# Kernel optimization log

Hardware: AMD Instinct MI355X
Metric: run time of the kernel (lower is better)

The kernel has to match this reference:

```python
import jax, jax.numpy as jnp
import numpy as np

N_NODES = 50000
N_EDGES = 640000
HID = 128


def _lin_params(key, out_dim, in_dim):
    kw, kb = jax.random.split(key)
    W = jax.random.normal(kw, (out_dim, in_dim), dtype=jnp.float32) * 0.02
    b = jax.random.normal(kb, (out_dim,), dtype=jnp.float32) * 0.02
    return W, b


def setup_inputs() -> dict:
    key = jax.random.key(0)
    ks = jax.random.split(key, 12)
    x = jax.random.normal(ks[0], (N_NODES, 3), dtype=jnp.float32)
    h = jax.random.normal(ks[1], (N_NODES, HID), dtype=jnp.float32)
    edge_index = jax.random.randint(ks[2], (2, N_EDGES), 0, N_NODES, dtype=jnp.int64)
    # edge_mlp: Linear(2H+1,H) -> SiLU -> Linear(H,H) -> SiLU -> Linear(H,H)
    ew1, eb1 = _lin_params(ks[3], HID, 2 * HID + 1)
    ew2, eb2 = _lin_params(ks[4], HID, HID)
    ew3, eb3 = _lin_params(ks[5], HID, HID)
    # coord_mlp: Linear(H,H) -> SiLU -> Linear(H,1)
    cw1, cb1 = _lin_params(ks[6], HID, HID)
    cw2, cb2 = _lin_params(ks[7], 1, HID)
    # node_mlp: Linear(2H,H) -> SiLU -> Linear(H,H) -> SiLU -> Linear(H,H)
    nw1, nb1 = _lin_params(ks[8], HID, 2 * HID)
    nw2, nb2 = _lin_params(ks[9], HID, HID)
    nw3, nb3 = _lin_params(ks[10], HID, HID)
    return {
        "x": x, "h": h, "edge_index": edge_index,
        "ew1": ew1, "eb1": eb1, "ew2": ew2, "eb2": eb2, "ew3": ew3, "eb3": eb3,
        "cw1": cw1, "cb1": cb1, "cw2": cw2, "cb2": cb2,
        "nw1": nw1, "nb1": nb1, "nw2": nw2, "nb2": nb2, "nw3": nw3, "nb3": nb3,
    }


def _lin(z, W, b):
    return z @ W.T + b


def _mlp3(z, W1, b1, W2, b2, W3, b3):
    z = jax.nn.silu(_lin(z, W1, b1))
    z = jax.nn.silu(_lin(z, W2, b2))
    return _lin(z, W3, b3)


def reference(x, h, edge_index,
              ew1, eb1, ew2, eb2, ew3, eb3,
              cw1, cb1, cw2, cb2,
              nw1, nb1, nw2, nb2, nw3, nb3):
    n = h.shape[0]
    src, dst = edge_index[0], edge_index[1]
    rel = x[src] - x[dst]                                   # [E, 3]
    d2 = jnp.sum(rel * rel, axis=-1, keepdims=True)         # [E, 1]
    e_in = jnp.concatenate([h[src], h[dst], d2], axis=-1)   # [E, 2H+1]
    m_ij = _mlp3(e_in, ew1, eb1, ew2, eb2, ew3, eb3)        # [E, H]
    m_aggr = jax.ops.segment_sum(m_ij, src, num_segments=n)  # [N, H]
    coord_coef = jnp.tanh(_lin(jax.nn.silu(_lin(m_ij, cw1, cb1)), cw2, cb2))  # [E, 1]
    delta_x = jax.ops.segment_sum(rel * coord_coef, src, num_segments=n)      # [N, 3]
    x_out = x + delta_x
    h_out = h + _mlp3(jnp.concatenate([h, m_aggr], axis=-1), nw1, nb1, nw2, nb2, nw3, nb3)
    return (x_out, h_out)
```

## Files before the change

kernel.cpp:

```cpp
#include <hip/hip_runtime.h>
#include <hip/hip_bf16.h>

#define N_NODES 50000
#define N_EDGES 640000
#define HID 128

typedef unsigned short ushort_t;
typedef __attribute__((ext_vector_type(8))) short bf16x8;
typedef __attribute__((ext_vector_type(4))) float f32x4;

#define U_MAGGR 0
#define U_HB    6400000
#define U_W1B   12800000
#define U_W2B   12832768
#define U_W3B   12849152
#define U_C1B   12865536
#define U_N1B   12881920
#define U_N2B   12914688
#define U_N3B   12931072
#define U_W1D2  12947456
#define U_WC    12947712
#define U_BC    12964096

__device__ __forceinline__ float silu_f(float v) {
    const float e = __builtin_amdgcn_exp2f(v * -1.442695041f);
    return v * __builtin_amdgcn_rcpf(1.0f + e);
}

__device__ __forceinline__ ushort_t f2b(float f) {
    __hip_bfloat16 b = __float2bfloat16(f);
    return __builtin_bit_cast(ushort_t, b);
}
__device__ __forceinline__ float b2f(ushort_t u) {
    union { float f; unsigned int i; } v; v.i = ((unsigned int)u) << 16; return v.f;
}
__device__ __forceinline__ float u2f(unsigned int u) {
    union { float f; unsigned int i; } v; v.i = u; return v.f;
}
__device__ __forceinline__ unsigned int pack2(float a, float b) {
    return (unsigned int)f2b(a) | ((unsigned int)f2b(b) << 16);
}
__device__ __forceinline__ void up8(const uint4& u, float* f) {
    f[0] = u2f(u.x << 16); f[1] = u2f(u.x & 0xffff0000u);
    f[2] = u2f(u.y << 16); f[3] = u2f(u.y & 0xffff0000u);
    f[4] = u2f(u.z << 16); f[5] = u2f(u.z & 0xffff0000u);
    f[6] = u2f(u.w << 16); f[7] = u2f(u.w & 0xffff0000u);
}
__device__ __forceinline__ void atom_add_f32(float* p, float v) { unsafeAtomicAdd(p, v); }

__device__ __forceinline__ void atom_pk_bf16(ushort_t* p, unsigned int v) {
#if __has_builtin(__builtin_amdgcn_global_atomic_fadd_v2bf16)
    typedef __attribute__((ext_vector_type(2))) short s2;
    s2 sv = __builtin_bit_cast(s2, v);
    __builtin_amdgcn_global_atomic_fadd_v2bf16((__attribute__((address_space(1))) s2*)p, sv);
#else
    unsigned int* up = (unsigned int*)p;
    unsigned int old = __hip_atomic_load(up, __ATOMIC_RELAXED, __HIP_MEMORY_SCOPE_AGENT), assumed;
    do {
        assumed = old;
        float lo = b2f((ushort_t)(assumed & 0xffff)) + b2f((ushort_t)(v & 0xffff));
        float hi = b2f((ushort_t)(assumed >> 16)) + b2f((ushort_t)(v >> 16));
        unsigned int nv = (unsigned int)f2b(lo) | ((unsigned int)f2b(hi) << 16);
        old = atomicCAS(up, assumed, nv);
    } while (old != assumed);
#endif
}

__global__ void prep_kernel(const float* __restrict__ x, const float* __restrict__ h,
                            const float* __restrict__ ew1, const float* __restrict__ ew2,
                            const float* __restrict__ ew3, const float* __restrict__ cw1,
                            const float* __restrict__ nw1, const float* __restrict__ nw2,
                            const float* __restrict__ nw3,
                            ushort_t* __restrict__ wsu, float* __restrict__ xout) {
    long i = (long)blockIdx.x * 256 + threadIdx.x;
    if (i < 3200000) { ((unsigned int*)(wsu + U_MAGGR))[i] = 0u; return; }
    i -= 3200000;
    if (i < 3200000) { ((unsigned int*)(wsu + U_HB))[i] = pack2(h[2 * i], h[2 * i + 1]); return; }
    i -= 3200000;
    if (i < 32768) {
        const int f = (int)(i >> 7);
        const int k = (int)(i & 127);
        const int src = (f < 128) ? (f * 257 + k) : ((f - 128) * 257 + 128 + k);
        wsu[U_W1B + i] = f2b(ew1[src]);
        return;
    }
    i -= 32768;
    if (i < 16384) { wsu[U_W2B + i] = f2b(ew2[i]); return; }
    i -= 16384;
    if (i < 16384) { wsu[U_W3B + i] = f2b(ew3[i]); return; }
    i -= 16384;
    if (i < 16384) { wsu[U_C1B + i] = f2b(cw1[i]); return; }
    i -= 16384;
    if (i < 32768) { wsu[U_N1B + i] = f2b(nw1[i]); return; }
    i -= 32768;
    if (i < 16384) { wsu[U_N2B + i] = f2b(nw2[i]); return; }
    i -= 16384;
    if (i < 16384) { wsu[U_N3B + i] = f2b(nw3[i]); return; }
    i -= 16384;
    if (i < 128) { ((float*)(wsu + U_W1D2))[i] = ew1[i * 257 + 256]; return; }
    i -= 128;
    if (i < 150000) xout[i] = x[i];
}

__global__ __launch_bounds__(256, 4) void ab_kernel(
    const ushort_t* __restrict__ hb, const ushort_t* __restrict__ wab,
    const float* __restrict__ eb1, ushort_t* __restrict__ abp,
    const ushort_t* __restrict__ c1b, const float* __restrict__ ew3,
    const float* __restrict__ eb3, const float* __restrict__ cb1,
    ushort_t* __restrict__ wcb, float* __restrict__ bcv, int nAB) {
    __shared__ ushort_t sH[16384];
    const int t = threadIdx.x;
    const int lane = t & 63;
    const int wid = t >> 6;
    const int r15 = lane & 15;
    const int khi = lane >> 4;
    const int rhi = khi * 4;

    if ((int)blockIdx.x == nAB) {
        for (int i = t; i < 16384; i += 256) {
            const int m = i >> 7, k = i & 127;
            sH[(k * 128 + m) ^ ((k & 7) << 3)] = f2b(ew3[i]);
        }
        __syncthreads();
#pragma unroll
        for (int kh = 0; kh < 2; ++kh) {
#pragma unroll
            for (int fi = 0; fi < 2; ++fi) {
                const int f0 = wid * 32 + fi * 16;
                const int kc = kh * 64;
                f32x4 acc[4];
#pragma unroll
                for (int ni = 0; ni < 4; ++ni) acc[ni] = (f32x4){0.f, 0.f, 0.f, 0.f};
#pragma unroll
                for (int ks = 0; ks < 4; ++ks) {
                    const bf16x8 a0 = *(const bf16x8*)(c1b + (f0 + r15) * 128 + ks * 32 + khi * 8);
                    bf16x8 b[4];
#pragma unroll
                    for (int ni = 0; ni < 4; ++ni) {
                        const int kk = kc + ni * 16 + r15;
                        b[ni] = *(const bf16x8*)(sH + ((kk * 128 + ks * 32 + khi * 8) ^ ((kk & 7) << 3)));
                    }
#pragma unroll
                    for (int ni = 0; ni < 4; ++ni)
                        acc[ni] = __builtin_amdgcn_mfma_f32_16x16x32_bf16(a0, b[ni], acc[ni], 0, 0, 0);
                }
#pragma unroll
                for (int ni = 0; ni < 4; ++ni) {
                    const int kk = kc + ni * 16 + r15;
#pragma unroll
                    for (int j = 0; j < 4; ++j)
                        wcb[(f0 + rhi + j) * 128 + kk] = f2b(acc[ni][j]);
                }
            }
        }
        {
            const int f = t >> 1, hf = t & 1;
            float s = 0.f;
            const int m0 = hf * 64;
#pragma unroll 8
            for (int m = m0; m < m0 + 64; ++m)
                s = fmaf(b2f(c1b[f * 128 + m]), eb3[m], s);
            s += __shfl_xor(s, 1);
            if (hf == 0) bcv[f] = cb1[f] + s;
        }
        return;
    }

    const int fb = wid * 64;
    const int n0 = blockIdx.x * 64;

    const uint4* hb4 = (const uint4*)hb;
#pragma unroll
    for (int it = 0; it < 4; ++it) {
        const int idx = it * 256 + t;
        const int e = idx >> 4, c = idx & 15;
        const int n = n0 + e;
        uint4 v = make_uint4(0u, 0u, 0u, 0u);
        if (n < N_NODES) v = hb4[(size_t)n * 16 + c];
        const int ui = (e * 128 + c * 8) ^ ((e & 7) << 3);
        *(uint4*)(sH + ui) = v;
    }
    __syncthreads();

    f32x4 acc[4][4];
#pragma unroll
    for (int mi = 0; mi < 4; ++mi)
#pragma unroll
        for (int ni = 0; ni < 4; ++ni) acc[mi][ni] = (f32x4){0.f, 0.f, 0.f, 0.f};
#pragma unroll
    for (int ks = 0; ks < 4; ++ks) {
        bf16x8 a[4];
#pragma unroll
        for (int mi = 0; mi < 4; ++mi)
            a[mi] = *(const bf16x8*)(wab + (fb + mi * 16 + r15) * 128 + ks * 32 + khi * 8);
        bf16x8 b[4];
#pragma unroll
        for (int ni = 0; ni < 4; ++ni) {
            const int e = ni * 16 + r15;
            const int ui = (e * 128 + ks * 32 + khi * 8) ^ ((e & 7) << 3);
            b[ni] = *(const bf16x8*)(sH + ui);
        }
#pragma unroll
        for (int mi = 0; mi < 4; ++mi)
#pragma unroll
            for (int ni = 0; ni < 4; ++ni)
                acc[mi][ni] = __builtin_amdgcn_mfma_f32_16x16x32_bf16(a[mi], b[ni], acc[mi][ni], 0, 0, 0);
    }

#pragma unroll
    for (int mi = 0; mi < 4; ++mi) {
        const int f0 = fb + mi * 16 + rhi;
        float4 bb = make_float4(0.f, 0.f, 0.f, 0.f);
        if (f0 >= 128) bb = *(const float4*)&eb1[f0 - 128];
#pragma unroll
        for (int ni = 0; ni < 4; ++ni) {
            const int n = n0 + ni * 16 + r15;
            if (n < N_NODES) {
                *(uint2*)(abp + (size_t)n * 256 + f0) =
                    make_uint2(pack2(acc[mi][ni][0] + bb.x, acc[mi][ni][1] + bb.y),
                               pack2(acc[mi][ni][2] + bb.z, acc[mi][ni][3] + bb.w));
            }
        }
    }
}

template <bool ACT>
__device__ __forceinline__ void dense128(ushort_t* sE, int srcBase, int dstBase,
                                         const ushort_t* __restrict__ W,
                                         const float* __restrict__ bias,
                                         int r15, int khi, int rhi, int fb) {
    f32x4 acc[4];
#pragma unroll
    for (int ni = 0; ni < 4; ++ni) acc[ni] = (f32x4){0.f, 0.f, 0.f, 0.f};
#pragma unroll
    for (int ks = 0; ks < 4; ++ks) {
        const bf16x8 a0 = *(const bf16x8*)(W + (fb + r15) * 128 + ks * 32 + khi * 8);
        bf16x8 b[4];
#pragma unroll
        for (int ni = 0; ni < 4; ++ni) {
            const int edge = ni * 16 + r15;
            const int ui = (srcBase + edge * 128 + ks * 32 + khi * 8) ^ ((edge & 7) << 3);
            b[ni] = *(const bf16x8*)(sE + ui);
        }
#pragma unroll
        for (int ni = 0; ni < 4; ++ni)
            acc[ni] = __builtin_amdgcn_mfma_f32_16x16x32_bf16(a0, b[ni], acc[ni], 0, 0, 0);
    }
    const float4 bb = *(const float4*)&bias[fb + rhi];
#pragma unroll
    for (int ni = 0; ni < 4; ++ni) {
        const int edge = ni * 16 + r15;
        float v0 = acc[ni][0] + bb.x;
        float v1 = acc[ni][1] + bb.y;
        float v2 = acc[ni][2] + bb.z;
        float v3 = acc[ni][3] + bb.w;
        if (ACT) { v0 = silu_f(v0); v1 = silu_f(v1); v2 = silu_f(v2); v3 = silu_f(v3); }
        const int ui = (dstBase + edge * 128 + fb + rhi) ^ ((edge & 7) << 3);
        *(uint2*)(sE + ui) = make_uint2(pack2(v0, v1), pack2(v2, v3));
    }
}

__global__ __launch_bounds__(512, 8) void edge_kernel(
    const float* __restrict__ x, const ushort_t* __restrict__ ab,
    const int* __restrict__ ei,
    const float* __restrict__ w1d2,
    const ushort_t* __restrict__ w2b, const float* __restrict__ eb2,
    const ushort_t* __restrict__ w3b, const float* __restrict__ eb3,
    const ushort_t* __restrict__ wcb, const float* __restrict__ bcv,
    const float* __restrict__ cw2, const float* __restrict__ cb2,
    float* __restrict__ xout, ushort_t* __restrict__ maggr) {
    __shared__ ushort_t sE[16384];
    __shared__ float srel[64][3];
    __shared__ float sd2[64];
    __shared__ int ssrc[64];
    __shared__ float sPart[8][64];

    const int t = threadIdx.x;
    const int lane = t & 63;
    const int wid = t >> 6;
    const int r15 = lane & 15;
    const int khi = lane >> 4;
    const int rhi = khi * 4;
    const int fb = wid * 16;
    const int e0 = blockIdx.x * 64;

    uint4 va[2], vb[2];
    int ui[2], ee[2];
    {
        const uint4* ab4 = (const uint4*)ab;
#pragma unroll
        for (int it = 0; it < 2; ++it) {
            const int idx = it * 512 + t;
            const int e = idx >> 4, c = idx & 15;
            const int s = ei[e0 + e];
            const int d = ei[N_EDGES + e0 + e];
            va[it] = ab4[(size_t)s * 32 + c];
            vb[it] = ab4[(size_t)d * 32 + 16 + c];
            ee[it] = e;
            ui[it] = (e * 128 + c * 8) ^ ((e & 7) << 3);
        }
    }
    if (t < 64) {
        const int s = ei[e0 + t], d = ei[N_EDGES + e0 + t];
        ssrc[t] = s;
        const float rx = x[3 * s] - x[3 * d];
        const float ry = x[3 * s + 1] - x[3 * d + 1];
        const float rz = x[3 * s + 2] - x[3 * d + 2];
        srel[t][0] = rx; srel[t][1] = ry; srel[t][2] = rz;
        sd2[t] = rx * rx + ry * ry + rz * rz;
    }
    __syncthreads();

#pragma unroll
    for (int it = 0; it < 2; ++it) {
        const int c8 = ((it * 512 + t) & 15) * 8;
        const float4 w0 = *(const float4*)&w1d2[c8];
        const float4 w1 = *(const float4*)&w1d2[c8 + 4];
        const float d2 = sd2[ee[it]];
        float fa[8], fbv[8];
        up8(va[it], fa);
        up8(vb[it], fbv);
        const float v0 = silu_f(fmaf(d2, w0.x, fa[0] + fbv[0]));
        const float v1 = silu_f(fmaf(d2, w0.y, fa[1] + fbv[1]));
        const float v2 = silu_f(fmaf(d2, w0.z, fa[2] + fbv[2]));
        const float v3 = silu_f(fmaf(d2, w0.w, fa[3] + fbv[3]));
        const float v4 = silu_f(fmaf(d2, w1.x, fa[4] + fbv[4]));
        const float v5 = silu_f(fmaf(d2, w1.y, fa[5] + fbv[5]));
        const float v6 = silu_f(fmaf(d2, w1.z, fa[6] + fbv[6]));
        const float v7 = silu_f(fmaf(d2, w1.w, fa[7] + fbv[7]));
        uint4 st;
        st.x = pack2(v0, v1); st.y = pack2(v2, v3);
        st.z = pack2(v4, v5); st.w = pack2(v6, v7);
        *(uint4*)(sE + ui[it]) = st;
    }
    __syncthreads();

    dense128<true>(sE, 0, 8192, w2b, eb2, r15, khi, rhi, fb);
    __syncthreads();

    dense128<false>(sE, 8192, 0, w3b, eb3, r15, khi, rhi, fb);

    {
        f32x4 acc[4];
#pragma unroll
        for (int ni = 0; ni < 4; ++ni) acc[ni] = (f32x4){0.f, 0.f, 0.f, 0.f};
#pragma unroll
        for (int ks = 0; ks < 4; ++ks) {
            const bf16x8 a0 = *(const bf16x8*)(wcb + (fb + r15) * 128 + ks * 32 + khi * 8);
            bf16x8 b[4];
#pragma unroll
            for (int ni = 0; ni < 4; ++ni) {
                const int edge = ni * 16 + r15;
                const int u = (8192 + edge * 128 + ks * 32 + khi * 8) ^ ((edge & 7) << 3);
                b[ni] = *(const bf16x8*)(sE + u);
            }
#pragma unroll
            for (int ni = 0; ni < 4; ++ni)
                acc[ni] = __builtin_amdgcn_mfma_f32_16x16x32_bf16(a0, b[ni], acc[ni], 0, 0, 0);
        }
        const float4 bb = *(const float4*)&bcv[fb + rhi];
        const float4 cw = *(const float4*)&cw2[fb + rhi];
        float p[4];
#pragma unroll
        for (int ni = 0; ni < 4; ++ni) {
            float s = silu_f(acc[ni][0] + bb.x) * cw.x;
            s = fmaf(silu_f(acc[ni][1] + bb.y), cw.y, s);
            s = fmaf(silu_f(acc[ni][2] + bb.z), cw.z, s);
            s = fmaf(silu_f(acc[ni][3] + bb.w), cw.w, s);
            p[ni] = s;
        }
#pragma unroll
        for (int ni = 0; ni < 4; ++ni) {
            p[ni] += __shfl_xor(p[ni], 16);
            p[ni] += __shfl_xor(p[ni], 32);
        }
        if (khi == 0) {
#pragma unroll
            for (int ni = 0; ni < 4; ++ni) sPart[wid][ni * 16 + r15] = p[ni];
        }
    }
    __syncthreads();

    {
        unsigned int v[8];
        size_t gaddr[8];
#pragma unroll
        for (int it = 0; it < 8; ++it) {
            const int idx = it * 512 + t;
            const int e = idx >> 6;
            const int dw = idx & 63;
            const int u = (e * 128 + dw * 2) ^ ((e & 7) << 3);
            v[it] = *(const unsigned int*)(sE + u);
            gaddr[it] = (size_t)ssrc[e] * 128 + dw * 2;
        }
#pragma unroll
        for (int it = 0; it < 8; ++it) atom_pk_bf16(maggr + gaddr[it], v[it]);
    }
    if (t < 64) {
        float s = sPart[0][t];
#pragma unroll
        for (int w = 1; w < 8; ++w) s += sPart[w][t];
        const float coef = tanhf(s + cb2[0]);
        const int sn = ssrc[t];
        atom_add_f32(&xout[3 * sn + 0], srel[t][0] * coef);
        atom_add_f32(&xout[3 * sn + 1], srel[t][1] * coef);
        atom_add_f32(&xout[3 * sn + 2], srel[t][2] * coef);
    }
}

__global__ __launch_bounds__(256, 4) void node_kernel(
    const float* __restrict__ h, const ushort_t* __restrict__ hb,
    const ushort_t* __restrict__ maggr,
    const ushort_t* __restrict__ n1b, const float* __restrict__ nb1,
    const ushort_t* __restrict__ n2b, const float* __restrict__ nb2,
    const ushort_t* __restrict__ n3b, const float* __restrict__ nb3,
    float* __restrict__ hout) {
    __shared__ ushort_t sE[16384];
    const int t = threadIdx.x;
    const int lane = t & 63;
    const int wid = t >> 6;
    const int r15 = lane & 15;
    const int khi = lane >> 4;
    const int rhi = khi * 4;
    const int fb = wid * 32;
    const int n0 = blockIdx.x * 64;

    const uint4* hb4 = (const uint4*)hb;
    const uint4* mg4 = (const uint4*)maggr;
#pragma unroll
    for (int it = 0; it < 8; ++it) {
        const int idx = it * 256 + t;
        const int e = idx >> 5, c = idx & 31;
        const int n = n0 + e;
        uint4 v = make_uint4(0u, 0u, 0u, 0u);
        if (n < N_NODES) v = (c < 16) ? hb4[(size_t)n * 16 + c] : mg4[(size_t)n * 16 + (c - 16)];
        const int ui = (e * 256 + c * 8) ^ ((e & 7) << 3);
        *(uint4*)(sE + ui) = v;
    }
    __syncthreads();

    f32x4 acc[2][4];
#pragma unroll
    for (int mi = 0; mi < 2; ++mi)
#pragma unroll
        for (int ni = 0; ni < 4; ++ni) acc[mi][ni] = (f32x4){0.f, 0.f, 0.f, 0.f};
#pragma unroll
    for (int ks = 0; ks < 8; ++ks) {
        const bf16x8 a0 = *(const bf16x8*)(n1b + (fb + r15) * 256 + ks * 32 + khi * 8);
        const bf16x8 a1 = *(const bf16x8*)(n1b + (fb + 16 + r15) * 256 + ks * 32 + khi * 8);
        bf16x8 b[4];
#pragma unroll
        for (int ni = 0; ni < 4; ++ni) {
            const int edge = ni * 16 + r15;
            const int ui = (edge * 256 + ks * 32 + khi * 8) ^ ((edge & 7) << 3);
            b[ni] = *(const bf16x8*)(sE + ui);
        }
#pragma unroll
        for (int ni = 0; ni < 4; ++ni) {
            acc[0][ni] = __builtin_amdgcn_mfma_f32_16x16x32_bf16(a0, b[ni], acc[0][ni], 0, 0, 0);
            acc[1][ni] = __builtin_amdgcn_mfma_f32_16x16x32_bf16(a1, b[ni], acc[1][ni], 0, 0, 0);
        }
    }
    __syncthreads();
    {
        const float4 bb0 = *(const float4*)&nb1[fb + rhi];
        const float4 bb1 = *(const float4*)&nb1[fb + 16 + rhi];
#pragma unroll
        for (int mi = 0; mi < 2; ++mi) {
            const float4 bb = mi ? bb1 : bb0;
#pragma unroll
            for (int ni = 0; ni < 4; ++ni) {
                const int edge = ni * 16 + r15;
                const float v0 = silu_f(acc[mi][ni][0] + bb.x);
                const float v1 = silu_f(acc[mi][ni][1] + bb.y);
                const float v2 = silu_f(acc[mi][ni][2] + bb.z);
                const float v3 = silu_f(acc[mi][ni][3] + bb.w);
                const int ui = (edge * 128 + fb + mi * 16 + rhi) ^ ((edge & 7) << 3);
                *(uint2*)(sE + ui) = make_uint2(pack2(v0, v1), pack2(v2, v3));
            }
        }
    }
    __syncthreads();

    {
#pragma unroll
        for (int half = 0; half < 2; ++half) {
            f32x4 a2[4];
#pragma unroll
            for (int ni = 0; ni < 4; ++ni) a2[ni] = (f32x4){0.f, 0.f, 0.f, 0.f};
            const int fbh = fb + half * 16;
#pragma unroll
            for (int ks = 0; ks < 4; ++ks) {
                const bf16x8 a0 = *(const bf16x8*)(n2b + (fbh + r15) * 128 + ks * 32 + khi * 8);
                bf16x8 b[4];
#pragma unroll
                for (int ni = 0; ni < 4; ++ni) {
                    const int edge = ni * 16 + r15;
                    const int ui = (edge * 128 + ks * 32 + khi * 8) ^ ((edge & 7) << 3);
                    b[ni] = *(const bf16x8*)(sE + ui);
                }
#pragma unroll
                for (int ni = 0; ni < 4; ++ni)
                    a2[ni] = __builtin_amdgcn_mfma_f32_16x16x32_bf16(a0, b[ni], a2[ni], 0, 0, 0);
            }
            const float4 bb = *(const float4*)&nb2[fbh + rhi];
#pragma unroll
            for (int ni = 0; ni < 4; ++ni) {
                const int edge = ni * 16 + r15;
                const float v0 = silu_f(a2[ni][0] + bb.x);
                const float v1 = silu_f(a2[ni][1] + bb.y);
                const float v2 = silu_f(a2[ni][2] + bb.z);
                const float v3 = silu_f(a2[ni][3] + bb.w);
                const int ui = (8192 + edge * 128 + fbh + rhi) ^ ((edge & 7) << 3);
                *(uint2*)(sE + ui) = make_uint2(pack2(v0, v1), pack2(v2, v3));
            }
        }
    }
    __syncthreads();

    {
        f32x4 a3[2][4];
#pragma unroll
        for (int mi = 0; mi < 2; ++mi)
#pragma unroll
            for (int ni = 0; ni < 4; ++ni) a3[mi][ni] = (f32x4){0.f, 0.f, 0.f, 0.f};
#pragma unroll
        for (int ks = 0; ks < 4; ++ks) {
            const bf16x8 a0 = *(const bf16x8*)(n3b + (fb + r15) * 128 + ks * 32 + khi * 8);
            const bf16x8 a1 = *(const bf16x8*)(n3b + (fb + 16 + r15) * 128 + ks * 32 + khi * 8);
            bf16x8 b[4];
#pragma unroll
            for (int ni = 0; ni < 4; ++ni) {
                const int edge = ni * 16 + r15;
                const int ui = (8192 + edge * 128 + ks * 32 + khi * 8) ^ ((edge & 7) << 3);
                b[ni] = *(const bf16x8*)(sE + ui);
            }
#pragma unroll
            for (int ni = 0; ni < 4; ++ni) {
                a3[0][ni] = __builtin_amdgcn_mfma_f32_16x16x32_bf16(a0, b[ni], a3[0][ni], 0, 0, 0);
                a3[1][ni] = __builtin_amdgcn_mfma_f32_16x16x32_bf16(a1, b[ni], a3[1][ni], 0, 0, 0);
            }
        }
        const float4 bb0 = *(const float4*)&nb3[fb + rhi];
        const float4 bb1 = *(const float4*)&nb3[fb + 16 + rhi];
#pragma unroll
        for (int mi = 0; mi < 2; ++mi) {
            const float4 bb = mi ? bb1 : bb0;
#pragma unroll
            for (int ni = 0; ni < 4; ++ni) {
                const int n = n0 + ni * 16 + r15;
                if (n < N_NODES) {
                    const size_t o = (size_t)n * 128 + fb + mi * 16 + rhi;
                    const float4 hv = *(const float4*)&h[o];
                    float4 ov;
                    ov.x = hv.x + a3[mi][ni][0] + bb.x;
                    ov.y = hv.y + a3[mi][ni][1] + bb.y;
                    ov.z = hv.z + a3[mi][ni][2] + bb.z;
                    ov.w = hv.w + a3[mi][ni][3] + bb.w;
                    *(float4*)&hout[o] = ov;
                }
            }
        }
    }
}

extern "C" void kernel_launch(void* const* d_in, const int* in_sizes, int n_in,
                              void* d_out, int out_size, void* d_ws, size_t ws_size,
                              hipStream_t stream) {
    const float* x   = (const float*)d_in[0];
    const float* h   = (const float*)d_in[1];
    const int*   ei  = (const int*)d_in[2];
    const float* ew1 = (const float*)d_in[3];
    const float* eb1 = (const float*)d_in[4];
    const float* ew2 = (const float*)d_in[5];
    const float* eb2 = (const float*)d_in[6];
    const float* ew3 = (const float*)d_in[7];
    const float* eb3 = (const float*)d_in[8];
    const float* cw1 = (const float*)d_in[9];
    const float* cb1 = (const float*)d_in[10];
    const float* cw2 = (const float*)d_in[11];
    const float* cb2 = (const float*)d_in[12];
    const float* nw1 = (const float*)d_in[13];
    const float* nb1 = (const float*)d_in[14];
    const float* nw2 = (const float*)d_in[15];
    const float* nb2 = (const float*)d_in[16];
    const float* nw3 = (const float*)d_in[17];
    const float* nb3 = (const float*)d_in[18];

    float* out  = (float*)d_out;
    float* xout = out;
    float* hout = out + (size_t)N_NODES * 3;
    ushort_t* wsu = (ushort_t*)d_ws;

    ushort_t* maggr = wsu + U_MAGGR;
    const ushort_t* hb  = wsu + U_HB;
    const ushort_t* wab = wsu + U_W1B;
    const ushort_t* w2b = wsu + U_W2B;
    const ushort_t* w3b = wsu + U_W3B;
    const ushort_t* c1b = wsu + U_C1B;
    const ushort_t* n1b = wsu + U_N1B;
    const ushort_t* n2b = wsu + U_N2B;
    const ushort_t* n3b = wsu + U_N3B;
    const float* w1d2 = (const float*)(wsu + U_W1D2);
    ushort_t* wcb = wsu + U_WC;
    float* bcv = (float*)(wsu + U_BC);

    ushort_t* abp = (ushort_t*)hout;

    const long prep_total = 3200000L + 3200000L + 32768 + 3 * 16384 + 32768 + 2 * 16384 + 128 + 150000;
    const int prep_blocks = (int)((prep_total + 255) / 256);
    prep_kernel<<<prep_blocks, 256, 0, stream>>>(x, h, ew1, ew2, ew3, cw1, nw1, nw2, nw3,
                                                 wsu, xout);

    const int nAB = (N_NODES + 63) / 64;
    ab_kernel<<<nAB + 1, 256, 0, stream>>>(hb, wab, eb1, abp,
                                           c1b, ew3, eb3, cb1, wcb, bcv, nAB);

    edge_kernel<<<N_EDGES / 64, 512, 0, stream>>>(x, abp, ei,
                                                  w1d2, w2b, eb2, w3b, eb3,
                                                  wcb, bcv, cw2, cb2,
                                                  xout, maggr);

    node_kernel<<<(N_NODES + 63) / 64, 256, 0, stream>>>(h, hb, maggr,
                                                         n1b, nb1, n2b, nb2, n3b, nb3,
                                                         hout);
}
```

Measured before the change: 316.1 us.

## Sort edges by source via counting sort and pre-reduce scatter atomics per block

Adds a counting sort of edges by source node: a histogram pass in prep, a single-block scan, and an atomic scatter kernel that builds source-sorted src/dst arrays. The edge kernel reads these sorted lists, so each block's 64 edges share few sources. It sums runs of equal sources locally before issuing bf16 and f32 atomics, which cuts atomic traffic into m_aggr and x_out. In exchange it adds three extra kernel launches and a memset. The single-block scan is serial, and the scatter's atomic placement makes edge order within a source nondeterministic.

```diff
diff --git a/kernel.cpp b/kernel.cpp
--- a/kernel.cpp
+++ b/kernel.cpp
@@ -21,6 +21,10 @@
 #define U_W1D2  12947456
 #define U_WC    12947712
 #define U_BC    12964096
+#define U_SRCS  12964352
+#define U_DSTS  14244352
+#define U_CNT   15524352
+#define U_PTR   15624448
 
 __device__ __forceinline__ float silu_f(float v) {
     const float e = __builtin_amdgcn_exp2f(v * -1.442695041f);
@@ -70,7 +74,7 @@
                             const float* __restrict__ ew1, const float* __restrict__ ew2,
                             const float* __restrict__ ew3, const float* __restrict__ cw1,
                             const float* __restrict__ nw1, const float* __restrict__ nw2,
-                            const float* __restrict__ nw3,
+                            const float* __restrict__ nw3, const int* __restrict__ ei,
                             ushort_t* __restrict__ wsu, float* __restrict__ xout) {
     long i = (long)blockIdx.x * 256 + threadIdx.x;
     if (i < 3200000) { ((unsigned int*)(wsu + U_MAGGR))[i] = 0u; return; }
@@ -99,7 +103,38 @@
     i -= 16384;
     if (i < 128) { ((float*)(wsu + U_W1D2))[i] = ew1[i * 257 + 256]; return; }
     i -= 128;
-    if (i < 150000) xout[i] = x[i];
+    if (i < 150000) { xout[i] = x[i]; return; }
+    i -= 150000;
+    if (i < N_EDGES) {
+        atomicAdd(((unsigned int*)(wsu + U_CNT)) + ei[i], 1u);
+    }
+}
+
+__global__ void scan_kernel(const unsigned int* __restrict__ cnt, unsigned int* __restrict__ ptr) {
+    __shared__ unsigned int sSum[256];
+    const int t = threadIdx.x;
+    const int lo = t * 196;
+    const int hi = (lo + 196 < N_NODES) ? lo + 196 : N_NODES;
+    unsigned int s = 0;
+    for (int i = lo; i < hi; ++i) s += cnt[i];
+    sSum[t] = s;
+    __syncthreads();
+    if (t == 0) {
+        unsigned int run = 0;
+        for (int i = 0; i < 256; ++i) { const unsigned int v = sSum[i]; sSum[i] = run; run += v; }
+    }
+    __syncthreads();
+    unsigned int off = sSum[t];
+    for (int i = lo; i < hi; ++i) { const unsigned int c = cnt[i]; ptr[i] = off; off += c; }
+}
+
+__global__ void scatter_kernel(const int* __restrict__ ei, unsigned int* __restrict__ ptr,
+                               int* __restrict__ srcs, int* __restrict__ dsts) {
+    const int e = blockIdx.x * 256 + threadIdx.x;
+    if (e >= N_EDGES) return;
+    const int s = ei[e], d = ei[N_EDGES + e];
+    const unsigned int pos = atomicAdd(&ptr[s], 1u);
+    srcs[pos] = s; dsts[pos] = d;
 }
 
 __global__ __launch_bounds__(256, 4) void ab_kernel(
@@ -262,7 +297,7 @@
 
 __global__ __launch_bounds__(512, 8) void edge_kernel(
     const float* __restrict__ x, const ushort_t* __restrict__ ab,
-    const int* __restrict__ ei,
+    const int* __restrict__ srcs, const int* __restrict__ dsts,
     const float* __restrict__ w1d2,
     const ushort_t* __restrict__ w2b, const float* __restrict__ eb2,
     const ushort_t* __restrict__ w3b, const float* __restrict__ eb3,
@@ -292,8 +327,8 @@
         for (int it = 0; it < 2; ++it) {
             const int idx = it * 512 + t;
             const int e = idx >> 4, c = idx & 15;
-            const int s = ei[e0 + e];
-            const int d = ei[N_EDGES + e0 + e];
+            const int s = srcs[e0 + e];
+            const int d = dsts[e0 + e];
             va[it] = ab4[(size_t)s * 32 + c];
             vb[it] = ab4[(size_t)d * 32 + 16 + c];
             ee[it] = e;
@@ -301,7 +336,7 @@
         }
     }
     if (t < 64) {
-        const int s = ei[e0 + t], d = ei[N_EDGES + e0 + t];
+        const int s = srcs[e0 + t], d = dsts[e0 + t];
         ssrc[t] = s;
         const float rx = x[3 * s] - x[3 * d];
         const float ry = x[3 * s + 1] - x[3 * d + 1];
@@ -381,30 +416,51 @@
     }
     __syncthreads();
 
-    {
-        unsigned int v[8];
-        size_t gaddr[8];
-#pragma unroll
-        for (int it = 0; it < 8; ++it) {
-            const int idx = it * 512 + t;
-            const int e = idx >> 6;
-            const int dw = idx & 63;
-            const int u = (e * 128 + dw * 2) ^ ((e & 7) << 3);
-            v[it] = *(const unsigned int*)(sE + u);
-            gaddr[it] = (size_t)ssrc[e] * 128 + dw * 2;
-        }
-#pragma unroll
-        for (int it = 0; it < 8; ++it) atom_pk_bf16(maggr + gaddr[it], v[it]);
-    }
     if (t < 64) {
         float s = sPart[0][t];
 #pragma unroll
         for (int w = 1; w < 8; ++w) s += sPart[w][t];
         const float coef = tanhf(s + cb2[0]);
-        const int sn = ssrc[t];
-        atom_add_f32(&xout[3 * sn + 0], srel[t][0] * coef);
-        atom_add_f32(&xout[3 * sn + 1], srel[t][1] * coef);
-        atom_add_f32(&xout[3 * sn + 2], srel[t][2] * coef);
+        sPart[0][t] = srel[t][0] * coef;
+        sPart[1][t] = srel[t][1] * coef;
+        sPart[2][t] = srel[t][2] * coef;
+    }
+
+    {
+        const int dw = t & 63;
+        const int rs = t >> 6;
+        float lo = 0.f, hi = 0.f;
+        int cur = ssrc[rs * 8];
+#pragma unroll
+        for (int j = 0; j < 8; ++j) {
+            const int e = rs * 8 + j;
+            const int s = ssrc[e];
+            if (s != cur) {
+                atom_pk_bf16(maggr + (size_t)cur * 128 + dw * 2, pack2(lo, hi));
+                lo = 0.f; hi = 0.f; cur = s;
+            }
+            const unsigned int v = *(const unsigned int*)(sE + ((e * 128 + dw * 2) ^ ((e & 7) << 3)));
+            lo += b2f((ushort_t)(v & 0xffff));
+            hi += b2f((ushort_t)(v >> 16));
+        }
+        atom_pk_bf16(maggr + (size_t)cur * 128 + dw * 2, pack2(lo, hi));
+    }
+    __syncthreads();
+
+    if (t < 64) {
+        const bool last = (t == 63) || (ssrc[t + 1] != ssrc[t]);
+        if (last) {
+            const int s = ssrc[t];
+            float ax = 0.f, ay = 0.f, az = 0.f;
+            int j = t;
+            while (j >= 0 && ssrc[j] == s) {
+                ax += sPart[0][j]; ay += sPart[1][j]; az += sPart[2][j];
+                --j;
+            }
+            atom_add_f32(&xout[3 * s + 0], ax);
+            atom_add_f32(&xout[3 * s + 1], ay);
+            atom_add_f32(&xout[3 * s + 2], az);
+        }
     }
 }
 
@@ -604,19 +660,28 @@
     const float* w1d2 = (const float*)(wsu + U_W1D2);
     ushort_t* wcb = wsu + U_WC;
     float* bcv = (float*)(wsu + U_BC);
+    int* srcs = (int*)(wsu + U_SRCS);
+    int* dsts = (int*)(wsu + U_DSTS);
+    unsigned int* cnt = (unsigned int*)(wsu + U_CNT);
+    unsigned int* ptr = (unsigned int*)(wsu + U_PTR);
 
     ushort_t* abp = (ushort_t*)hout;
 
-    const long prep_total = 3200000L + 3200000L + 32768 + 3 * 16384 + 32768 + 2 * 16384 + 128 + 150000;
+    hipMemsetAsync(cnt, 0, 50048 * sizeof(unsigned int), stream);
+
+    const long prep_total = 3200000L + 3200000L + 32768 + 3 * 16384 + 32768 + 2 * 16384 + 128 + 150000 + N_EDGES;
     const int prep_blocks = (int)((prep_total + 255) / 256);
     prep_kernel<<<prep_blocks, 256, 0, stream>>>(x, h, ew1, ew2, ew3, cw1, nw1, nw2, nw3,
-                                                 wsu, xout);
+                                                 ei, wsu, xout);
+
+    scan_kernel<<<1, 256, 0, stream>>>(cnt, ptr);
+    scatter_kernel<<<(N_EDGES + 255) / 256, 256, 0, stream>>>(ei, ptr, srcs, dsts);
 
     const int nAB = (N_NODES + 63) / 64;
     ab_kernel<<<nAB + 1, 256, 0, stream>>>(hb, wab, eb1, abp,
                                            c1b, ew3, eb3, cb1, wcb, bcv, nAB);
 
-    edge_kernel<<<N_EDGES / 64, 512, 0, stream>>>(x, abp, ei,
+    edge_kernel<<<N_EDGES / 64, 512, 0, stream>>>(x, abp, srcs, dsts,
                                                   w1d2, w2b, eb2, w3b, eb3,
                                                   wcb, bcv, cw2, cb2,
                                                   xout, maggr);
```

Measured after the change: 388.4 us. +22.9%, slower.
